# Optimization experiments

Measured on AMD Instinct MI355X. Metric: run time of the kernel, lower is better.

## Reference

```python
import jax, jax.numpy as jnp
import numpy as np

NUM_HEADS = 8
NEG_INF = -1e9  # stand-in for -inf in the causal mask (avoids nan under masked softmax)


def setup_inputs() -> dict:
    key = jax.random.key(0)
    ks = jax.random.split(key, 8)
    B, C, H, W = 2, 512, 64, 64
    E = 512
    s = 1.0 / np.sqrt(C)
    return {
        "query": jax.random.normal(ks[0], (B, C, H, W), jnp.float32),
        "key": jax.random.normal(ks[1], (B, C, H, W), jnp.float32),
        "Wq": jax.random.normal(ks[2], (E, C), jnp.float32) * s,
        "bq": jax.random.normal(ks[3], (E,), jnp.float32) * 0.01,
        "Wk": jax.random.normal(ks[4], (E, C), jnp.float32) * s,
        "bk": jax.random.normal(ks[5], (E,), jnp.float32) * 0.01,
        "Wv": jax.random.normal(ks[6], (E, C), jnp.float32) * s,
        "bv": jax.random.normal(ks[7], (E,), jnp.float32) * 0.01,
    }


def reference(query, key, Wq, bq, Wk, bk, Wv, bv):
    B, qdim, H, W = query.shape
    N = H * W
    E = Wq.shape[0]
    nh = NUM_HEADS
    hd = E // nh

    # (B, C, H, W) -> (B, N, C)
    q_tok = query.transpose(0, 2, 3, 1).reshape(B, N, qdim)
    k_tok = key.transpose(0, 2, 3, 1).reshape(B, N, key.shape[1])

    q = (q_tok @ Wq.T + bq).reshape(B, N, nh, hd)
    k = (k_tok @ Wk.T + bk).reshape(B, N, nh, hd)
    v = (k_tok @ Wv.T + bv).reshape(B, N, nh, hd)

    # scores: (B, heads, N, N)
    scores = jnp.einsum("bqhd,bkhd->bhqk", q, k) / jnp.sqrt(jnp.float32(hd))
    causal = jnp.tril(jnp.ones((N, N), dtype=bool))
    scores = jnp.where(causal, scores, NEG_INF)
    attn = jax.nn.softmax(scores, axis=-1)  # dropout p=0.0 -> identity

    x = jnp.einsum("bhqk,bkhd->bhqd", attn, v)  # (B, h, N, hd)
    # permute to (B, h, hd, N) then view as (B, E, H, W) — matches torch ordering
    out = x.transpose(0, 1, 3, 2).reshape(B, E, H, W)
    return out
```

## Files before the change

### kernel.cpp

```cpp
#include <hip/hip_runtime.h>


typedef __bf16 bf16;
typedef __attribute__((ext_vector_type(8))) __bf16 bf16x8;
typedef __attribute__((ext_vector_type(4))) float floatx4;

#define B_ 2
#define Cc 512
#define Nn 4096
#define Ee 512
#define NH 8
#define HD 64

#define QSCALE 0.1803368801111204f

__global__ __launch_bounds__(64) void detect_dtype(
    const unsigned short* __restrict__ w, int* __restrict__ flag) {
  bool bad = false;
#pragma unroll
  for (int i = 0; i < 16; ++i) {
    unsigned u = w[threadIdx.x * 16 + i];
    float v = __uint_as_float(u << 16);
    bad |= !(v > -1024.f && v < 1024.f);
  }
  unsigned long long b = __ballot(bad);
  if (threadIdx.x == 0) *flag = (b != 0ull) ? 1 : 0;
}

#define WSEG 262144
#define WTOT 787968
__global__ __launch_bounds__(256) void wcvt(
    const float* __restrict__ Wq, const float* __restrict__ Wk,
    const float* __restrict__ Wv, const float* __restrict__ bq,
    const float* __restrict__ bk, const float* __restrict__ bv,
    bf16* __restrict__ out, const int* __restrict__ flagp) {
  if (!*flagp) return;
  int idx = (blockIdx.x * 256 + threadIdx.x) * 8;
  if (idx >= WTOT) return;
  const float* src;
  int off;
  if (idx < WSEG)            { src = Wq; off = idx; }
  else if (idx < 2 * WSEG)   { src = Wk; off = idx - WSEG; }
  else if (idx < 3 * WSEG)   { src = Wv; off = idx - 2 * WSEG; }
  else if (idx < 3 * WSEG + 512)  { src = bq; off = idx - 3 * WSEG; }
  else if (idx < 3 * WSEG + 1024) { src = bk; off = idx - 3 * WSEG - 512; }
  else                            { src = bv; off = idx - 3 * WSEG - 1024; }
  float4 a = *(const float4*)(src + off);
  float4 c = *(const float4*)(src + off + 4);
  union { bf16 h[8]; bf16x8 v; } u;
  u.h[0] = (bf16)a.x; u.h[1] = (bf16)a.y; u.h[2] = (bf16)a.z; u.h[3] = (bf16)a.w;
  u.h[4] = (bf16)c.x; u.h[5] = (bf16)c.y; u.h[6] = (bf16)c.z; u.h[7] = (bf16)c.w;
  *(bf16x8*)(out + idx) = u.v;
}

__device__ __forceinline__ bf16x8 load8e(const void* base, size_t eidx, int f32) {
  if (!f32) return *(const bf16x8*)((const bf16*)base + eidx);
  const float* f = (const float*)base + eidx;
  float4 a = *(const float4*)f;
  float4 c = *(const float4*)(f + 4);
  union { bf16 h[8]; bf16x8 v; } u;
  u.h[0] = (bf16)a.x; u.h[1] = (bf16)a.y; u.h[2] = (bf16)a.z; u.h[3] = (bf16)a.w;
  u.h[4] = (bf16)c.x; u.h[5] = (bf16)c.y; u.h[6] = (bf16)c.z; u.h[7] = (bf16)c.w;
  return u.v;
}

__global__ __launch_bounds__(256) void transpose_k(
    const void* __restrict__ X0, const void* __restrict__ X1,
    bf16* __restrict__ T0, bf16* __restrict__ T1,
    const int* __restrict__ flagp) {
  const int f32 = *flagp;
  __shared__ __align__(16) bf16 T[64 * 64];
  const int z = blockIdx.z;
  const int bb = z & 1;
  const void* src = (z >> 1) ? X1 : X0;
  bf16* dst = (z >> 1) ? T1 : T0;
  const int n0 = blockIdx.x * 64, c0 = blockIdx.y * 64;
  const int t = threadIdx.x;
  const size_t sbase = ((size_t)bb * Cc + c0) * (size_t)Nn + n0;

#pragma unroll
  for (int it = 0; it < 2; ++it) {
    int task = t + it * 256;
    int crow = task >> 3, gr = task & 7;
    bf16x8 v = load8e(src, sbase + (size_t)crow * Nn + gr * 8, f32);
    int slot = gr ^ (crow & 7);
    *(bf16x8*)&T[crow * 64 + slot * 8] = v;
  }
  __syncthreads();
  const int nrow = t & 63, cp = t >> 6;
  bf16* db = dst + ((size_t)bb * Nn + n0 + nrow) * Cc + c0;
#pragma unroll
  for (int it = 0; it < 2; ++it) {
    int cg = cp * 2 + it;
    union { bf16 h[8]; bf16x8 v; } u;
#pragma unroll
    for (int j = 0; j < 8; ++j) {
      int c = cg * 8 + j;
      int slot = (nrow >> 3) ^ (c & 7);
      u.h[j] = T[c * 64 + slot * 8 + (nrow & 7)];
    }
    *(bf16x8*)(db + cg * 8) = u.v;
  }
}

__global__ __launch_bounds__(256) void gemm3(
    const bf16* __restrict__ Xtq, const bf16* __restrict__ Xtk,
    const void* __restrict__ Wq0, const bf16* __restrict__ Wqb,
    const void* __restrict__ Wk0, const bf16* __restrict__ Wkb,
    const void* __restrict__ Wv0, const bf16* __restrict__ Wvb,
    const void* __restrict__ bq0, const bf16* __restrict__ bqb,
    const void* __restrict__ bk0, const bf16* __restrict__ bkb,
    const void* __restrict__ bv0, const bf16* __restrict__ bvb,
    bf16* __restrict__ Qt, bf16* __restrict__ Kt, bf16* __restrict__ Vh,
    int zoff, const int* __restrict__ flagp) {
  const int f32 = *flagp;
  const int z = (int)blockIdx.z + zoff;
  const int op = z >> 1, b = z & 1;
  const bf16 *A, *Bt, *bias;
  bf16* Out;
  long sAb, sBb, sOb;
  int Nq, biasOnM, m0, n0;
  float scaleOut;
  if (op == 0) {
    A = Xtq; sAb = (long)Nn * Cc;
    Bt = f32 ? Wqb : (const bf16*)Wq0; sBb = 0;
    bias = f32 ? bqb : (const bf16*)bq0;
    Out = Qt; sOb = (long)Nn * Ee; Nq = Ee; biasOnM = 0; scaleOut = QSCALE;
    m0 = blockIdx.x * 128; n0 = blockIdx.y * 64;
  } else if (op == 1) {
    A = Xtk; sAb = (long)Nn * Cc;
    Bt = f32 ? Wkb : (const bf16*)Wk0; sBb = 0;
    bias = f32 ? bkb : (const bf16*)bk0;
    Out = Kt; sOb = (long)Nn * Ee; Nq = Ee; biasOnM = 0; scaleOut = 1.0f;
    m0 = blockIdx.x * 128; n0 = blockIdx.y * 64;
  } else {
    A = f32 ? Wvb : (const bf16*)Wv0; sAb = 0;
    Bt = Xtk; sBb = (long)Nn * Cc;
    bias = f32 ? bvb : (const bf16*)bv0;
    Out = Vh; sOb = (long)Ee * Nn; Nq = Nn; biasOnM = 1; scaleOut = 1.0f;
    m0 = (blockIdx.x >> 3) * 128;
    n0 = (blockIdx.y * 8 + (blockIdx.x & 7)) * 64;
  }
  constexpr int K = 512;
  constexpr int SA = 40;
  __shared__ __align__(16) bf16 As[2][128 * SA];
  __shared__ __align__(16) bf16 Bs[2][64 * SA];
  const int tid = threadIdx.x;
  const int lane = tid & 63, wave = tid >> 6;
  const int quad = lane >> 4, lm = lane & 15;
  const bf16* Ab = A + (size_t)b * sAb;
  const bf16* Bb = Bt + (size_t)b * sBb;
  bf16* Ob = Out + (size_t)b * sOb;

  const int arow = tid >> 2, ag = tid & 3;

  floatx4 acc[2][4];
#pragma unroll
  for (int i = 0; i < 2; ++i)
#pragma unroll
    for (int j = 0; j < 4; ++j) acc[i][j] = (floatx4){0.f, 0.f, 0.f, 0.f};

  bf16x8 a0 = *(const bf16x8*)(Ab + (size_t)(m0 + arow) * K + ag * 8);
  bf16x8 a1 = *(const bf16x8*)(Ab + (size_t)(m0 + 64 + arow) * K + ag * 8);
  bf16x8 b0 = *(const bf16x8*)(Bb + (size_t)(n0 + arow) * K + ag * 8);
  *(bf16x8*)&As[0][arow * SA + ag * 8] = a0;
  *(bf16x8*)&As[0][(64 + arow) * SA + ag * 8] = a1;
  *(bf16x8*)&Bs[0][arow * SA + ag * 8] = b0;
  __syncthreads();

  for (int kk = 0; kk < 16; ++kk) {
    const int c = kk & 1;
    const bool more = kk < 15;
    if (more) {
      int k0 = (kk + 1) * 32;
      a0 = *(const bf16x8*)(Ab + (size_t)(m0 + arow) * K + k0 + ag * 8);
      a1 = *(const bf16x8*)(Ab + (size_t)(m0 + 64 + arow) * K + k0 + ag * 8);
      b0 = *(const bf16x8*)(Bb + (size_t)(n0 + arow) * K + k0 + ag * 8);
    }
    bf16x8 af[2], bfr[4];
#pragma unroll
    for (int mf = 0; mf < 2; ++mf) {
      int r = wave * 32 + mf * 16 + lm;
      af[mf] = *(const bf16x8*)&As[c][r * SA + quad * 8];
    }
#pragma unroll
    for (int nf = 0; nf < 4; ++nf) {
      int r = nf * 16 + lm;
      bfr[nf] = *(const bf16x8*)&Bs[c][r * SA + quad * 8];
    }
    if (more) {
      *(bf16x8*)&As[c ^ 1][arow * SA + ag * 8] = a0;
      *(bf16x8*)&As[c ^ 1][(64 + arow) * SA + ag * 8] = a1;
      *(bf16x8*)&Bs[c ^ 1][arow * SA + ag * 8] = b0;
    }
#pragma unroll
    for (int mf = 0; mf < 2; ++mf)
#pragma unroll
      for (int nf = 0; nf < 4; ++nf)
        acc[mf][nf] = __builtin_amdgcn_mfma_f32_16x16x32_bf16(
            af[mf], bfr[nf], acc[mf][nf], 0, 0, 0);
    __syncthreads();
  }

#pragma unroll
  for (int mf = 0; mf < 2; ++mf) {
#pragma unroll
    for (int nf = 0; nf < 4; ++nf) {
      int col = n0 + nf * 16 + lm;
      float bn = biasOnM ? 0.f : (float)bias[col];
#pragma unroll
      for (int r = 0; r < 4; ++r) {
        int rowg = m0 + wave * 32 + mf * 16 + quad * 4 + r;
        float bv = biasOnM ? (float)bias[rowg] : bn;
        Ob[(size_t)rowg * Nq + col] = (bf16)((acc[mf][nf][r] + bv) * scaleOut);
      }
    }
  }
}

__device__ __forceinline__ float fast_exp2(float x) {
  return __builtin_amdgcn_exp2f(x);
}
__device__ __forceinline__ unsigned pack_bf16_2(float a, float b) {
  unsigned ua = __float_as_uint(a) + 0x8000u;
  unsigned ub = __float_as_uint(b) + 0x8000u;
  return (ua >> 16) | (ub & 0xFFFF0000u);
}

__global__ __launch_bounds__(256, 4) void attn(
    const bf16* __restrict__ Qt, const bf16* __restrict__ Kt,
    const bf16* __restrict__ Ve, void* __restrict__ Out,
    const int* __restrict__ flagp) {
  const int f32 = *flagp;
  constexpr int SK = 72;
  __shared__ __align__(16) bf16 Ks[2][64 * SK];
  __shared__ __align__(16) bf16 Vs[2][64 * SK];
  const int tid = threadIdx.x, lane = tid & 63, w = tid >> 6;
  const int quad = lane >> 4, lm = lane & 15;

  const int L = (int)blockIdx.x + 64 * (int)blockIdx.y + 512 * (int)blockIdx.z;
  const int xcd = L & 7, slot0 = L >> 3;
  const int half = slot0 >> 6, sp = slot0 & 63;
  const int p = half ? 63 - sp : sp;
  const int hp = xcd * 2 + half;
  const int b = hp >> 3, h = hp & 7;

  const int Q0 = p * 64;
  const int qbase = Q0 + w * 16;
  const int last = p;

  bf16x8 qf[2];
  {
    const bf16* qp =
        Qt + ((size_t)b * Nn + qbase + lm) * Ee + h * HD + quad * 8;
    qf[0] = *(const bf16x8*)qp;
    qf[1] = *(const bf16x8*)(qp + 32);
  }
  floatx4 accO[4];
#pragma unroll
  for (int df = 0; df < 4; ++df) accO[df] = (floatx4){0.f, 0.f, 0.f, 0.f};
  float lsum = 0.f;

  const int r0 = tid >> 3, g = tid & 7;
  const int sslot = ((g + r0) & 7) * 8;
  const bf16* kp0 = Kt + ((size_t)b * Nn + r0) * Ee + h * HD + g * 8;
  const bf16* kp1 = kp0 + (size_t)32 * Ee;
  const bf16* vp0 = Ve + ((size_t)b * Ee + h * HD + r0) * Nn + g * 8;
  const bf16* vp1 = vp0 + (size_t)32 * Nn;

  const int rbase = ((lm >> 2) << 3) | (lm & 3);

  bf16x8 ka[2], kb[2], va[2], vb[2];
#define LOADT(s)                                                   \
  do {                                                             \
    ka[s] = *(const bf16x8*)kp0; kb[s] = *(const bf16x8*)kp1;      \
    va[s] = *(const bf16x8*)vp0; vb[s] = *(const bf16x8*)vp1;      \
    kp0 += (size_t)64 * Ee; kp1 += (size_t)64 * Ee;                \
    vp0 += 64; vp1 += 64;                                          \
  } while (0)
#define STAGET(s, buf)                                             \
  do {                                                             \
    *(bf16x8*)&Ks[buf][r0 * SK + sslot] = ka[s];                   \
    *(bf16x8*)&Ks[buf][(r0 + 32) * SK + sslot] = kb[s];            \
    *(bf16x8*)&Vs[buf][r0 * SK + sslot] = va[s];                   \
    *(bf16x8*)&Vs[buf][(r0 + 32) * SK + sslot] = vb[s];            \
  } while (0)

  LOADT(0);
  if (last >= 1) LOADT(1);
  STAGET(0, 0);
  __syncthreads();

#pragma unroll 1
  for (int kt = 0; kt <= last; kt += 2) {
#pragma unroll
    for (int u = 0; u < 2; ++u) {
      const int t = kt + u;
      if (u == 1 && t > last) break;
      const int k0 = t * 64;
      if (t + 2 <= last) LOADT(u);
      const bool skip = k0 > qbase + 15;

      bf16x8 pb[2];
      if (!skip) {
        floatx4 accS[4];
#pragma unroll
        for (int f = 0; f < 4; ++f) accS[f] = (floatx4){0.f, 0.f, 0.f, 0.f};
        __builtin_amdgcn_s_setprio(1);
#pragma unroll
        for (int ks = 0; ks < 2; ++ks)
#pragma unroll
          for (int f = 0; f < 4; ++f) {
            const int R = rbase + ((f & 1) << 2) + ((f >> 1) << 5);
            const int sl = (ks * 4 + quad + R) & 7;
            bf16x8 ak = *(const bf16x8*)&Ks[u][R * SK + sl * 8];
            accS[f] = __builtin_amdgcn_mfma_f32_16x16x32_bf16(
                ak, qf[ks], accS[f], 0, 0, 0);
          }
        __builtin_amdgcn_s_setprio(0);
        const bool maskt = (k0 + 63 > qbase);
        if (!maskt) {
          float la = 0.f, lb = 0.f;
#pragma unroll
          for (int g2 = 0; g2 < 2; ++g2) {
            union { unsigned pk[4]; bf16x8 v; } uu;
#pragma unroll
            for (int jp = 0; jp < 4; ++jp) {
              const int fidx = g2 * 2 + (jp >> 1);
              const int re = (jp & 1) * 2;
              float p0 = fast_exp2(accS[fidx][re]);
              float p1 = fast_exp2(accS[fidx][re + 1]);
              la += p0; lb += p1;
              uu.pk[jp] = pack_bf16_2(p0, p1);
            }
            pb[g2] = uu.v;
          }
          lsum += la + lb;
        } else {
          const int qg = qbase + lm;
          float la = 0.f, lb = 0.f;
#pragma unroll
          for (int g2 = 0; g2 < 2; ++g2) {
            union { unsigned pk[4]; bf16x8 v; } uu;
#pragma unroll
            for (int jp = 0; jp < 4; ++jp) {
              const int fidx = g2 * 2 + (jp >> 1);
              const int re = (jp & 1) * 2;
              const int key0 = k0 + g2 * 32 + quad * 8 + jp * 2;
              float p0 = fast_exp2(accS[fidx][re]);
              float p1 = fast_exp2(accS[fidx][re + 1]);
              if (key0 > qg) p0 = 0.f;
              if (key0 + 1 > qg) p1 = 0.f;
              la += p0; lb += p1;
              uu.pk[jp] = pack_bf16_2(p0, p1);
            }
            pb[g2] = uu.v;
          }
          lsum += la + lb;
        }
      }
      if (t + 1 <= last) STAGET(u ^ 1, u ^ 1);
      if (!skip) {
        __builtin_amdgcn_s_setprio(1);
#pragma unroll
        for (int g2 = 0; g2 < 2; ++g2)
#pragma unroll
          for (int df = 0; df < 4; ++df) {
            const int Rv = df * 16 + lm;
            const int sl = (g2 * 4 + quad + Rv) & 7;
            bf16x8 av = *(const bf16x8*)&Vs[u][Rv * SK + sl * 8];
            accO[df] = __builtin_amdgcn_mfma_f32_16x16x32_bf16(
                av, pb[g2], accO[df], 0, 0, 0);
          }
        __builtin_amdgcn_s_setprio(0);
      }
      __syncthreads();
    }
  }
#undef LOADT
#undef STAGET

  lsum += __shfl_xor(lsum, 16);
  lsum += __shfl_xor(lsum, 32);

  const float inv = 1.0f / lsum;
  const int qg = qbase + lm;
#pragma unroll
  for (int df = 0; df < 4; ++df) {
#pragma unroll
    for (int r = 0; r < 4; ++r) {
      int d = h * HD + df * 16 + quad * 4 + r;
      size_t off = ((size_t)b * Ee + d) * Nn + qg;
      if (!f32) ((bf16*)Out)[off] = (bf16)(accO[df][r] * inv);
      else      ((float*)Out)[off] = accO[df][r] * inv;
    }
  }
}

extern "C" void kernel_launch(void* const* d_in, const int* in_sizes, int n_in,
                              void* d_out, int out_size, void* d_ws,
                              size_t ws_size, hipStream_t stream) {
  const void* q  = d_in[0];
  const void* k  = d_in[1];
  const void* Wq = d_in[2];
  const void* bq = d_in[3];
  const void* Wk = d_in[4];
  const void* bk = d_in[5];
  const void* Wv = d_in[6];
  const void* bv = d_in[7];

  const size_t SZ = (size_t)B_ * Nn * Cc;
  int*  flag = (int*)d_ws;
  bf16* Xtq  = (bf16*)((char*)d_ws + 1024);
  bf16* Qt   = Xtq + SZ;
  bf16* Kt   = Qt + SZ;
  bf16* Xtk  = (bf16*)d_out;
  bf16* Vh   = Xtq;
  bf16* Wb   = (bf16*)((char*)d_out + 8 * 1024 * 1024);
  bf16* Wqb = Wb,            *Wkb = Wb + WSEG,    *Wvb = Wb + 2 * WSEG;
  bf16* bqb = Wb + 3 * WSEG, *bkb = bqb + 512,    *bvb = bqb + 1024;

  detect_dtype<<<1, 64, 0, stream>>>((const unsigned short*)Wq, flag);
  wcvt<<<(WTOT / 8 + 255) / 256, 256, 0, stream>>>(
      (const float*)Wq, (const float*)Wk, (const float*)Wv,
      (const float*)bq, (const float*)bk, (const float*)bv, Wb, flag);
  transpose_k<<<dim3(64, 8, 4), 256, 0, stream>>>(q, k, Xtq, Xtk, flag);
  gemm3<<<dim3(32, 8, 4), 256, 0, stream>>>(
      Xtq, Xtk, Wq, Wqb, Wk, Wkb, Wv, Wvb,
      bq, bqb, bk, bkb, bv, bvb, Qt, Kt, Vh, 0, flag);
  gemm3<<<dim3(32, 8, 2), 256, 0, stream>>>(
      Xtq, Xtk, Wq, Wqb, Wk, Wkb, Wv, Wvb,
      bq, bqb, bk, bkb, bv, bvb, Qt, Kt, Vh, 4, flag);
  attn<<<dim3(64, NH, B_), 256, 0, stream>>>(Qt, Kt, Vh, d_out, flag);
}
```

Baseline: 191.6 us.

## Load V fragments directly from global into registers, drop V shared-memory staging

The attention kernel no longer stages V tiles through double-buffered shared memory. Each wave now loads its own V MFMA operands straight from global memory into registers at the start of each key tile. This removes the LDS writes and reads for V and halves shared memory use, which may allow higher occupancy. In exchange, each of the four waves redundantly fetches the full V tile from global/L2, and the load latency is only partly hidden by the QK and softmax work.

```diff
diff --git a/kernel.cpp b/kernel.cpp
--- a/kernel.cpp
+++ b/kernel.cpp
@@ -234,7 +234,6 @@
   const int f32 = *flagp;
   constexpr int SK = 72;
   __shared__ __align__(16) bf16 Ks[2][64 * SK];
-  __shared__ __align__(16) bf16 Vs[2][64 * SK];
   const int tid = threadIdx.x, lane = tid & 63, w = tid >> 6;
   const int quad = lane >> 4, lm = lane & 15;
 
@@ -265,30 +264,29 @@
   const int sslot = ((g + r0) & 7) * 8;
   const bf16* kp0 = Kt + ((size_t)b * Nn + r0) * Ee + h * HD + g * 8;
   const bf16* kp1 = kp0 + (size_t)32 * Ee;
-  const bf16* vp0 = Ve + ((size_t)b * Ee + h * HD + r0) * Nn + g * 8;
-  const bf16* vp1 = vp0 + (size_t)32 * Nn;
+
+  const bf16* vr0 = Ve + ((size_t)b * Ee + h * HD + lm) * Nn + quad * 8;
+  const bf16* vr1 = vr0 + (size_t)16 * Nn;
+  const bf16* vr2 = vr0 + (size_t)32 * Nn;
+  const bf16* vr3 = vr0 + (size_t)48 * Nn;
 
   const int rbase = ((lm >> 2) << 3) | (lm & 3);
 
-  bf16x8 ka[2], kb[2], va[2], vb[2];
-#define LOADT(s)                                                   \
+  bf16x8 ka[2], kb[2];
+#define LOADK(s)                                                   \
   do {                                                             \
     ka[s] = *(const bf16x8*)kp0; kb[s] = *(const bf16x8*)kp1;      \
-    va[s] = *(const bf16x8*)vp0; vb[s] = *(const bf16x8*)vp1;      \
     kp0 += (size_t)64 * Ee; kp1 += (size_t)64 * Ee;                \
-    vp0 += 64; vp1 += 64;                                          \
   } while (0)
-#define STAGET(s, buf)                                             \
+#define STAGEK(s, buf)                                             \
   do {                                                             \
     *(bf16x8*)&Ks[buf][r0 * SK + sslot] = ka[s];                   \
     *(bf16x8*)&Ks[buf][(r0 + 32) * SK + sslot] = kb[s];            \
-    *(bf16x8*)&Vs[buf][r0 * SK + sslot] = va[s];                   \
-    *(bf16x8*)&Vs[buf][(r0 + 32) * SK + sslot] = vb[s];            \
   } while (0)
 
-  LOADT(0);
-  if (last >= 1) LOADT(1);
-  STAGET(0, 0);
+  LOADK(0);
+  if (last >= 1) LOADK(1);
+  STAGEK(0, 0);
   __syncthreads();
 
 #pragma unroll 1
@@ -298,8 +296,18 @@
       const int t = kt + u;
       if (u == 1 && t > last) break;
       const int k0 = t * 64;
-      if (t + 2 <= last) LOADT(u);
       const bool skip = k0 > qbase + 15;
+
+      bf16x8 av0, av1, av2, av3, av4, av5, av6, av7;
+      if (!skip) {
+        av0 = *(const bf16x8*)(vr0);        av1 = *(const bf16x8*)(vr0 + 32);
+        av2 = *(const bf16x8*)(vr1);        av3 = *(const bf16x8*)(vr1 + 32);
+        av4 = *(const bf16x8*)(vr2);        av5 = *(const bf16x8*)(vr2 + 32);
+        av6 = *(const bf16x8*)(vr3);        av7 = *(const bf16x8*)(vr3 + 32);
+      }
+      vr0 += 64; vr1 += 64; vr2 += 64; vr3 += 64;
+
+      if (t + 2 <= last) LOADK(u);
 
       bf16x8 pb[2];
       if (!skip) {
@@ -359,26 +367,24 @@
           lsum += la + lb;
         }
       }
-      if (t + 1 <= last) STAGET(u ^ 1, u ^ 1);
+      if (t + 1 <= last) STAGEK(u ^ 1, u ^ 1);
       if (!skip) {
         __builtin_amdgcn_s_setprio(1);
-#pragma unroll
-        for (int g2 = 0; g2 < 2; ++g2)
-#pragma unroll
-          for (int df = 0; df < 4; ++df) {
-            const int Rv = df * 16 + lm;
-            const int sl = (g2 * 4 + quad + Rv) & 7;
-            bf16x8 av = *(const bf16x8*)&Vs[u][Rv * SK + sl * 8];
-            accO[df] = __builtin_amdgcn_mfma_f32_16x16x32_bf16(
-                av, pb[g2], accO[df], 0, 0, 0);
-          }
+        accO[0] = __builtin_amdgcn_mfma_f32_16x16x32_bf16(av0, pb[0], accO[0], 0, 0, 0);
+        accO[1] = __builtin_amdgcn_mfma_f32_16x16x32_bf16(av2, pb[0], accO[1], 0, 0, 0);
+        accO[2] = __builtin_amdgcn_mfma_f32_16x16x32_bf16(av4, pb[0], accO[2], 0, 0, 0);
+        accO[3] = __builtin_amdgcn_mfma_f32_16x16x32_bf16(av6, pb[0], accO[3], 0, 0, 0);
+        accO[0] = __builtin_amdgcn_mfma_f32_16x16x32_bf16(av1, pb[1], accO[0], 0, 0, 0);
+        accO[1] = __builtin_amdgcn_mfma_f32_16x16x32_bf16(av3, pb[1], accO[1], 0, 0, 0);
+        accO[2] = __builtin_amdgcn_mfma_f32_16x16x32_bf16(av5, pb[1], accO[2], 0, 0, 0);
+        accO[3] = __builtin_amdgcn_mfma_f32_16x16x32_bf16(av7, pb[1], accO[3], 0, 0, 0);
         __builtin_amdgcn_s_setprio(0);
       }
       __syncthreads();
     }
   }
-#undef LOADT
-#undef STAGET
+#undef LOADK
+#undef STAGEK
 
   lsum += __shfl_xor(lsum, 16);
   lsum += __shfl_xor(lsum, 32);
```

Measured after the change: 266.3 us. 1.39x slower.

## Software-pipeline QK^T one tile ahead of softmax and PV in attention

Applied to the files above, without the earlier changes.

Restructures the causal attention loop so the score MFMAs for tile t+1 are issued before the exp and PV MFMAs of tile t, using two score accumulator sets. K is staged two tiles ahead and V one tile ahead, with clamped prefetch indices so loads run unconditionally. It also drops the per-wave skip check for fully masked tiles. The aim is to overlap MFMA work with the exp/pack ALU work and to hide memory latency, at the cost of more registers and possibly lower occupancy.

```diff
diff --git a/kernel.cpp b/kernel.cpp
--- a/kernel.cpp
+++ b/kernel.cpp
@@ -227,6 +227,89 @@
   return (ua >> 16) | (ub & 0xFFFF0000u);
 }
 
+#define TCLMP(tt) ((tt) > 63 ? 63 : (tt))
+
+#define ATTN_STEP(t_, u_, CUR, NXT)                                          \
+  {                                                                          \
+       \
+    *(bf16x8*)&Ks[(u_)][r0 * SK + sslot] = ka[(u_)];                         \
+    *(bf16x8*)&Ks[(u_)][(r0 + 32) * SK + sslot] = kb[(u_)];                  \
+    *(bf16x8*)&Vs[(u_) ^ 1][r0 * SK + sslot] = va[(u_)];                     \
+    *(bf16x8*)&Vs[(u_) ^ 1][(r0 + 32) * SK + sslot] = vb[(u_)];              \
+                                       \
+    ka[(u_)] = *(const bf16x8*)(kp0 + (size_t)TCLMP((t_) + 4) * (64 * Ee));  \
+    kb[(u_)] = *(const bf16x8*)(kp1 + (size_t)TCLMP((t_) + 4) * (64 * Ee));  \
+    va[(u_)] = *(const bf16x8*)(vp0 + TCLMP((t_) + 3) * 64);                 \
+    vb[(u_)] = *(const bf16x8*)(vp1 + TCLMP((t_) + 3) * 64);                 \
+                 \
+    if ((t_) < last) {                                                       \
+      _Pragma("unroll") for (int f = 0; f < 4; ++f)                          \
+          NXT[f] = (floatx4){0.f, 0.f, 0.f, 0.f};                            \
+      __builtin_amdgcn_s_setprio(1);                                         \
+      _Pragma("unroll") for (int ks2 = 0; ks2 < 2; ++ks2) {                  \
+        _Pragma("unroll") for (int f = 0; f < 4; ++f) {                      \
+          const int R = rbase + ((f & 1) << 2) + ((f >> 1) << 5);            \
+          const int sl = (ks2 * 4 + quad + R) & 7;                           \
+          bf16x8 ak = *(const bf16x8*)&Ks[(u_) ^ 1][R * SK + sl * 8];        \
+          NXT[f] = __builtin_amdgcn_mfma_f32_16x16x32_bf16(                  \
+              ak, qf[ks2], NXT[f], 0, 0, 0);                                 \
+        }                                                                    \
+      }                                                                      \
+      __builtin_amdgcn_s_setprio(0);                                         \
+    }                                                                        \
+                        \
+    bf16x8 pb[2];                                                            \
+    if ((t_) != last) {                                                      \
+      float la = 0.f, lb = 0.f;                                              \
+      _Pragma("unroll") for (int g2 = 0; g2 < 2; ++g2) {                     \
+        union { unsigned pk[4]; bf16x8 v; } uu;                              \
+        _Pragma("unroll") for (int jp = 0; jp < 4; ++jp) {                   \
+          const int fidx = g2 * 2 + (jp >> 1);                               \
+          const int re = (jp & 1) * 2;                                       \
+          float p0 = fast_exp2(CUR[fidx][re]);                               \
+          float p1 = fast_exp2(CUR[fidx][re + 1]);                           \
+          la += p0; lb += p1;                                                \
+          uu.pk[jp] = pack_bf16_2(p0, p1);                                   \
+        }                                                                    \
+        pb[g2] = uu.v;                                                       \
+      }                                                                      \
+      lsum += la + lb;                                                       \
+    } else {                                                                 \
+      const int qgm = qbase + lm;                                            \
+      const int k0b = (t_) * 64;                                             \
+      float la = 0.f, lb = 0.f;                                              \
+      _Pragma("unroll") for (int g2 = 0; g2 < 2; ++g2) {                     \
+        union { unsigned pk[4]; bf16x8 v; } uu;                              \
+        _Pragma("unroll") for (int jp = 0; jp < 4; ++jp) {                   \
+          const int fidx = g2 * 2 + (jp >> 1);                               \
+          const int re = (jp & 1) * 2;                                       \
+          const int key0 = k0b + g2 * 32 + quad * 8 + jp * 2;                \
+          float p0 = fast_exp2(CUR[fidx][re]);                               \
+          float p1 = fast_exp2(CUR[fidx][re + 1]);                           \
+          if (key0 > qgm) p0 = 0.f;                                          \
+          if (key0 + 1 > qgm) p1 = 0.f;                                      \
+          la += p0; lb += p1;                                                \
+          uu.pk[jp] = pack_bf16_2(p0, p1);                                   \
+        }                                                                    \
+        pb[g2] = uu.v;                                                       \
+      }                                                                      \
+      lsum += la + lb;                                                       \
+    }                                                                        \
+                                                       \
+    __builtin_amdgcn_s_setprio(1);                                           \
+    _Pragma("unroll") for (int g2 = 0; g2 < 2; ++g2) {                       \
+      _Pragma("unroll") for (int df = 0; df < 4; ++df) {                     \
+        const int Rv = df * 16 + lm;                                         \
+        const int sl = (g2 * 4 + quad + Rv) & 7;                             \
+        bf16x8 av = *(const bf16x8*)&Vs[(u_)][Rv * SK + sl * 8];             \
+        accO[df] = __builtin_amdgcn_mfma_f32_16x16x32_bf16(                  \
+            av, pb[g2], accO[df], 0, 0, 0);                                  \
+      }                                                                      \
+    }                                                                        \
+    __builtin_amdgcn_s_setprio(0);                                           \
+    __syncthreads();                                                         \
+  }
+
 __global__ __launch_bounds__(256, 4) void attn(
     const bf16* __restrict__ Qt, const bf16* __restrict__ Kt,
     const bf16* __restrict__ Ve, void* __restrict__ Out,
@@ -245,8 +328,7 @@
   const int hp = xcd * 2 + half;
   const int b = hp >> 3, h = hp & 7;
 
-  const int Q0 = p * 64;
-  const int qbase = Q0 + w * 16;
+  const int qbase = p * 64 + w * 16;
   const int last = p;
 
   bf16x8 qf[2];
@@ -271,114 +353,54 @@
   const int rbase = ((lm >> 2) << 3) | (lm & 3);
 
   bf16x8 ka[2], kb[2], va[2], vb[2];
-#define LOADT(s)                                                   \
-  do {                                                             \
-    ka[s] = *(const bf16x8*)kp0; kb[s] = *(const bf16x8*)kp1;      \
-    va[s] = *(const bf16x8*)vp0; vb[s] = *(const bf16x8*)vp1;      \
-    kp0 += (size_t)64 * Ee; kp1 += (size_t)64 * Ee;                \
-    vp0 += 64; vp1 += 64;                                          \
-  } while (0)
-#define STAGET(s, buf)                                             \
-  do {                                                             \
-    *(bf16x8*)&Ks[buf][r0 * SK + sslot] = ka[s];                   \
-    *(bf16x8*)&Ks[buf][(r0 + 32) * SK + sslot] = kb[s];            \
-    *(bf16x8*)&Vs[buf][r0 * SK + sslot] = va[s];                   \
-    *(bf16x8*)&Vs[buf][(r0 + 32) * SK + sslot] = vb[s];            \
-  } while (0)
-
-  LOADT(0);
-  if (last >= 1) LOADT(1);
-  STAGET(0, 0);
+
+  ka[0] = *(const bf16x8*)kp0;
+  kb[0] = *(const bf16x8*)kp1;
+  ka[1] = *(const bf16x8*)(kp0 + (size_t)64 * Ee);
+  kb[1] = *(const bf16x8*)(kp1 + (size_t)64 * Ee);
+  va[0] = *(const bf16x8*)vp0;
+  vb[0] = *(const bf16x8*)vp1;
+  *(bf16x8*)&Ks[0][r0 * SK + sslot] = ka[0];
+  *(bf16x8*)&Ks[0][(r0 + 32) * SK + sslot] = kb[0];
+  *(bf16x8*)&Ks[1][r0 * SK + sslot] = ka[1];
+  *(bf16x8*)&Ks[1][(r0 + 32) * SK + sslot] = kb[1];
+  *(bf16x8*)&Vs[0][r0 * SK + sslot] = va[0];
+  *(bf16x8*)&Vs[0][(r0 + 32) * SK + sslot] = vb[0];
+  ka[0] = *(const bf16x8*)(kp0 + (size_t)2 * 64 * Ee);
+  kb[0] = *(const bf16x8*)(kp1 + (size_t)2 * 64 * Ee);
+  ka[1] = *(const bf16x8*)(kp0 + (size_t)3 * 64 * Ee);
+  kb[1] = *(const bf16x8*)(kp1 + (size_t)3 * 64 * Ee);
+  va[0] = *(const bf16x8*)(vp0 + 1 * 64);
+  vb[0] = *(const bf16x8*)(vp1 + 1 * 64);
+  va[1] = *(const bf16x8*)(vp0 + 2 * 64);
+  vb[1] = *(const bf16x8*)(vp1 + 2 * 64);
   __syncthreads();
+
+  floatx4 accSA[4], accSB[4];
+#pragma unroll
+  for (int f = 0; f < 4; ++f) {
+    accSA[f] = (floatx4){0.f, 0.f, 0.f, 0.f};
+    accSB[f] = (floatx4){0.f, 0.f, 0.f, 0.f};
+  }
+  __builtin_amdgcn_s_setprio(1);
+#pragma unroll
+  for (int ks2 = 0; ks2 < 2; ++ks2) {
+#pragma unroll
+    for (int f = 0; f < 4; ++f) {
+      const int R = rbase + ((f & 1) << 2) + ((f >> 1) << 5);
+      const int sl = (ks2 * 4 + quad + R) & 7;
+      bf16x8 ak = *(const bf16x8*)&Ks[0][R * SK + sl * 8];
+      accSA[f] = __builtin_amdgcn_mfma_f32_16x16x32_bf16(
+          ak, qf[ks2], accSA[f], 0, 0, 0);
+    }
+  }
+  __builtin_amdgcn_s_setprio(0);
 
 #pragma unroll 1
   for (int kt = 0; kt <= last; kt += 2) {
-#pragma unroll
-    for (int u = 0; u < 2; ++u) {
-      const int t = kt + u;
-      if (u == 1 && t > last) break;
-      const int k0 = t * 64;
-      if (t + 2 <= last) LOADT(u);
-      const bool skip = k0 > qbase + 15;
-
-      bf16x8 pb[2];
-      if (!skip) {
-        floatx4 accS[4];
-#pragma unroll
-        for (int f = 0; f < 4; ++f) accS[f] = (floatx4){0.f, 0.f, 0.f, 0.f};
-        __builtin_amdgcn_s_setprio(1);
-#pragma unroll
-        for (int ks = 0; ks < 2; ++ks)
-#pragma unroll
-          for (int f = 0; f < 4; ++f) {
-            const int R = rbase + ((f & 1) << 2) + ((f >> 1) << 5);
-            const int sl = (ks * 4 + quad + R) & 7;
-            bf16x8 ak = *(const bf16x8*)&Ks[u][R * SK + sl * 8];
-            accS[f] = __builtin_amdgcn_mfma_f32_16x16x32_bf16(
-                ak, qf[ks], accS[f], 0, 0, 0);
-          }
-        __builtin_amdgcn_s_setprio(0);
-        const bool maskt = (k0 + 63 > qbase);
-        if (!maskt) {
-          float la = 0.f, lb = 0.f;
-#pragma unroll
-          for (int g2 = 0; g2 < 2; ++g2) {
-            union { unsigned pk[4]; bf16x8 v; } uu;
-#pragma unroll
-            for (int jp = 0; jp < 4; ++jp) {
-              const int fidx = g2 * 2 + (jp >> 1);
-              const int re = (jp & 1) * 2;
-              float p0 = fast_exp2(accS[fidx][re]);
-              float p1 = fast_exp2(accS[fidx][re + 1]);
-              la += p0; lb += p1;
-              uu.pk[jp] = pack_bf16_2(p0, p1);
-            }
-            pb[g2] = uu.v;
-          }
-          lsum += la + lb;
-        } else {
-          const int qg = qbase + lm;
-          float la = 0.f, lb = 0.f;
-#pragma unroll
-          for (int g2 = 0; g2 < 2; ++g2) {
-            union { unsigned pk[4]; bf16x8 v; } uu;
-#pragma unroll
-            for (int jp = 0; jp < 4; ++jp) {
-              const int fidx = g2 * 2 + (jp >> 1);
-              const int re = (jp & 1) * 2;
-              const int key0 = k0 + g2 * 32 + quad * 8 + jp * 2;
-              float p0 = fast_exp2(accS[fidx][re]);
-              float p1 = fast_exp2(accS[fidx][re + 1]);
-              if (key0 > qg) p0 = 0.f;
-              if (key0 + 1 > qg) p1 = 0.f;
-              la += p0; lb += p1;
-              uu.pk[jp] = pack_bf16_2(p0, p1);
-            }
-            pb[g2] = uu.v;
-          }
-          lsum += la + lb;
-        }
-      }
-      if (t + 1 <= last) STAGET(u ^ 1, u ^ 1);
-      if (!skip) {
-        __builtin_amdgcn_s_setprio(1);
-#pragma unroll
-        for (int g2 = 0; g2 < 2; ++g2)
-#pragma unroll
-          for (int df = 0; df < 4; ++df) {
-            const int Rv = df * 16 + lm;
-            const int sl = (g2 * 4 + quad + Rv) & 7;
-            bf16x8 av = *(const bf16x8*)&Vs[u][Rv * SK + sl * 8];
-            accO[df] = __builtin_amdgcn_mfma_f32_16x16x32_bf16(
-                av, pb[g2], accO[df], 0, 0, 0);
-          }
-        __builtin_amdgcn_s_setprio(0);
-      }
-      __syncthreads();
-    }
-  }
-#undef LOADT
-#undef STAGET
+    ATTN_STEP(kt, 0, accSA, accSB);
+    if (kt + 1 <= last) ATTN_STEP(kt + 1, 1, accSB, accSA);
+  }
 
   lsum += __shfl_xor(lsum, 16);
   lsum += __shfl_xor(lsum, 32);
```

Result: slower. 255.6 us (+33.4%).

## Fuse weight conversion into transpose, merge projection GEMMs, deepen GEMM prefetch

Applied to the files above, without the earlier changes.

Folds the weight/bias bf16 conversion into the input-transpose kernel as an extra grid slice, so one launch replaces two. When the workspace is large enough, V gets its own buffer instead of aliasing the transposed query, which lets all three projections run in a single GEMM launch. The GEMM main loop now prefetches global tiles two steps ahead using register double-buffering. These changes cut launch and serialization overhead and hide more load latency, at the cost of extra registers and workspace memory.

```diff
diff --git a/kernel.cpp b/kernel.cpp
--- a/kernel.cpp
+++ b/kernel.cpp
@@ -29,29 +29,6 @@
 
 #define WSEG 262144
 #define WTOT 787968
-__global__ __launch_bounds__(256) void wcvt(
-    const float* __restrict__ Wq, const float* __restrict__ Wk,
-    const float* __restrict__ Wv, const float* __restrict__ bq,
-    const float* __restrict__ bk, const float* __restrict__ bv,
-    bf16* __restrict__ out, const int* __restrict__ flagp) {
-  if (!*flagp) return;
-  int idx = (blockIdx.x * 256 + threadIdx.x) * 8;
-  if (idx >= WTOT) return;
-  const float* src;
-  int off;
-  if (idx < WSEG)            { src = Wq; off = idx; }
-  else if (idx < 2 * WSEG)   { src = Wk; off = idx - WSEG; }
-  else if (idx < 3 * WSEG)   { src = Wv; off = idx - 2 * WSEG; }
-  else if (idx < 3 * WSEG + 512)  { src = bq; off = idx - 3 * WSEG; }
-  else if (idx < 3 * WSEG + 1024) { src = bk; off = idx - 3 * WSEG - 512; }
-  else                            { src = bv; off = idx - 3 * WSEG - 1024; }
-  float4 a = *(const float4*)(src + off);
-  float4 c = *(const float4*)(src + off + 4);
-  union { bf16 h[8]; bf16x8 v; } u;
-  u.h[0] = (bf16)a.x; u.h[1] = (bf16)a.y; u.h[2] = (bf16)a.z; u.h[3] = (bf16)a.w;
-  u.h[4] = (bf16)c.x; u.h[5] = (bf16)c.y; u.h[6] = (bf16)c.z; u.h[7] = (bf16)c.w;
-  *(bf16x8*)(out + idx) = u.v;
-}
 
 __device__ __forceinline__ bf16x8 load8e(const void* base, size_t eidx, int f32) {
   if (!f32) return *(const bf16x8*)((const bf16*)base + eidx);
@@ -64,11 +41,35 @@
   return u.v;
 }
 
-__global__ __launch_bounds__(256) void transpose_k(
+__global__ __launch_bounds__(256) void prep(
     const void* __restrict__ X0, const void* __restrict__ X1,
     bf16* __restrict__ T0, bf16* __restrict__ T1,
-    const int* __restrict__ flagp) {
+    const float* __restrict__ Wq, const float* __restrict__ Wk,
+    const float* __restrict__ Wv, const float* __restrict__ bq,
+    const float* __restrict__ bk, const float* __restrict__ bv,
+    bf16* __restrict__ Wb, const int* __restrict__ flagp) {
   const int f32 = *flagp;
+  if (blockIdx.z == 4) {
+    if (!f32) return;
+    int task = (int)blockIdx.y * 64 + (int)blockIdx.x;
+    int idx = (task * 256 + (int)threadIdx.x) * 8;
+    if (idx >= WTOT) return;
+    const float* src;
+    int off;
+    if (idx < WSEG)            { src = Wq; off = idx; }
+    else if (idx < 2 * WSEG)   { src = Wk; off = idx - WSEG; }
+    else if (idx < 3 * WSEG)   { src = Wv; off = idx - 2 * WSEG; }
+    else if (idx < 3 * WSEG + 512)  { src = bq; off = idx - 3 * WSEG; }
+    else if (idx < 3 * WSEG + 1024) { src = bk; off = idx - 3 * WSEG - 512; }
+    else                            { src = bv; off = idx - 3 * WSEG - 1024; }
+    float4 a = *(const float4*)(src + off);
+    float4 c = *(const float4*)(src + off + 4);
+    union { bf16 h[8]; bf16x8 v; } u;
+    u.h[0] = (bf16)a.x; u.h[1] = (bf16)a.y; u.h[2] = (bf16)a.z; u.h[3] = (bf16)a.w;
+    u.h[4] = (bf16)c.x; u.h[5] = (bf16)c.y; u.h[6] = (bf16)c.z; u.h[7] = (bf16)c.w;
+    *(bf16x8*)(Wb + idx) = u.v;
+    return;
+  }
   __shared__ __align__(16) bf16 T[64 * 64];
   const int z = blockIdx.z;
   const int bb = z & 1;
@@ -160,47 +161,54 @@
 #pragma unroll
     for (int j = 0; j < 4; ++j) acc[i][j] = (floatx4){0.f, 0.f, 0.f, 0.f};
 
-  bf16x8 a0 = *(const bf16x8*)(Ab + (size_t)(m0 + arow) * K + ag * 8);
-  bf16x8 a1 = *(const bf16x8*)(Ab + (size_t)(m0 + 64 + arow) * K + ag * 8);
-  bf16x8 b0 = *(const bf16x8*)(Bb + (size_t)(n0 + arow) * K + ag * 8);
-  *(bf16x8*)&As[0][arow * SA + ag * 8] = a0;
-  *(bf16x8*)&As[0][(64 + arow) * SA + ag * 8] = a1;
-  *(bf16x8*)&Bs[0][arow * SA + ag * 8] = b0;
+  bf16x8 pa0[2], pa1[2], pb0[2];
+#define LOADG(s, step)                                                      \
+  do {                                                                      \
+    const int k0_ = (step) * 32;                                            \
+    pa0[s] = *(const bf16x8*)(Ab + (size_t)(m0 + arow) * K + k0_ + ag * 8); \
+    pa1[s] = *(const bf16x8*)(Ab + (size_t)(m0 + 64 + arow) * K + k0_ + ag * 8); \
+    pb0[s] = *(const bf16x8*)(Bb + (size_t)(n0 + arow) * K + k0_ + ag * 8); \
+  } while (0)
+#define STAGEG(s, c_)                                                       \
+  do {                                                                      \
+    *(bf16x8*)&As[c_][arow * SA + ag * 8] = pa0[s];                         \
+    *(bf16x8*)&As[c_][(64 + arow) * SA + ag * 8] = pa1[s];                  \
+    *(bf16x8*)&Bs[c_][arow * SA + ag * 8] = pb0[s];                         \
+  } while (0)
+
+  LOADG(0, 0);
+  LOADG(1, 1);
+  STAGEG(0, 0);
   __syncthreads();
 
-  for (int kk = 0; kk < 16; ++kk) {
-    const int c = kk & 1;
-    const bool more = kk < 15;
-    if (more) {
-      int k0 = (kk + 1) * 32;
-      a0 = *(const bf16x8*)(Ab + (size_t)(m0 + arow) * K + k0 + ag * 8);
-      a1 = *(const bf16x8*)(Ab + (size_t)(m0 + 64 + arow) * K + k0 + ag * 8);
-      b0 = *(const bf16x8*)(Bb + (size_t)(n0 + arow) * K + k0 + ag * 8);
+  for (int kk = 0; kk < 16; kk += 2) {
+#pragma unroll
+    for (int u = 0; u < 2; ++u) {
+      const int t = kk + u;
+      if (t + 2 < 16) LOADG(u, t + 2);
+      bf16x8 af[2], bfr[4];
+#pragma unroll
+      for (int mf = 0; mf < 2; ++mf) {
+        int r = wave * 32 + mf * 16 + lm;
+        af[mf] = *(const bf16x8*)&As[u][r * SA + quad * 8];
+      }
+#pragma unroll
+      for (int nf = 0; nf < 4; ++nf) {
+        int r = nf * 16 + lm;
+        bfr[nf] = *(const bf16x8*)&Bs[u][r * SA + quad * 8];
+      }
+      if (t + 1 < 16) STAGEG(u ^ 1, u ^ 1);
+#pragma unroll
+      for (int mf = 0; mf < 2; ++mf)
+#pragma unroll
+        for (int nf = 0; nf < 4; ++nf)
+          acc[mf][nf] = __builtin_amdgcn_mfma_f32_16x16x32_bf16(
+              af[mf], bfr[nf], acc[mf][nf], 0, 0, 0);
+      __syncthreads();
     }
-    bf16x8 af[2], bfr[4];
-#pragma unroll
-    for (int mf = 0; mf < 2; ++mf) {
-      int r = wave * 32 + mf * 16 + lm;
-      af[mf] = *(const bf16x8*)&As[c][r * SA + quad * 8];
-    }
-#pragma unroll
-    for (int nf = 0; nf < 4; ++nf) {
-      int r = nf * 16 + lm;
-      bfr[nf] = *(const bf16x8*)&Bs[c][r * SA + quad * 8];
-    }
-    if (more) {
-      *(bf16x8*)&As[c ^ 1][arow * SA + ag * 8] = a0;
-      *(bf16x8*)&As[c ^ 1][(64 + arow) * SA + ag * 8] = a1;
-      *(bf16x8*)&Bs[c ^ 1][arow * SA + ag * 8] = b0;
-    }
-#pragma unroll
-    for (int mf = 0; mf < 2; ++mf)
-#pragma unroll
-      for (int nf = 0; nf < 4; ++nf)
-        acc[mf][nf] = __builtin_amdgcn_mfma_f32_16x16x32_bf16(
-            af[mf], bfr[nf], acc[mf][nf], 0, 0, 0);
-    __syncthreads();
-  }
+  }
+#undef LOADG
+#undef STAGEG
 
 #pragma unroll
   for (int mf = 0; mf < 2; ++mf) {
@@ -415,21 +423,30 @@
   bf16* Qt   = Xtq + SZ;
   bf16* Kt   = Qt + SZ;
   bf16* Xtk  = (bf16*)d_out;
-  bf16* Vh   = Xtq;
   bf16* Wb   = (bf16*)((char*)d_out + 8 * 1024 * 1024);
   bf16* Wqb = Wb,            *Wkb = Wb + WSEG,    *Wvb = Wb + 2 * WSEG;
   bf16* bqb = Wb + 3 * WSEG, *bkb = bqb + 512,    *bvb = bqb + 1024;
 
+  const size_t need = 1024 + 4 * SZ * sizeof(bf16);
+  const bool sep = ws_size >= need;
+  bf16* Vh = sep ? (Kt + SZ) : Xtq;
+
   detect_dtype<<<1, 64, 0, stream>>>((const unsigned short*)Wq, flag);
-  wcvt<<<(WTOT / 8 + 255) / 256, 256, 0, stream>>>(
+  prep<<<dim3(64, 8, 5), 256, 0, stream>>>(
+      q, k, Xtq, Xtk,
       (const float*)Wq, (const float*)Wk, (const float*)Wv,
       (const float*)bq, (const float*)bk, (const float*)bv, Wb, flag);
-  transpose_k<<<dim3(64, 8, 4), 256, 0, stream>>>(q, k, Xtq, Xtk, flag);
-  gemm3<<<dim3(32, 8, 4), 256, 0, stream>>>(
-      Xtq, Xtk, Wq, Wqb, Wk, Wkb, Wv, Wvb,
-      bq, bqb, bk, bkb, bv, bvb, Qt, Kt, Vh, 0, flag);
-  gemm3<<<dim3(32, 8, 2), 256, 0, stream>>>(
-      Xtq, Xtk, Wq, Wqb, Wk, Wkb, Wv, Wvb,
-      bq, bqb, bk, bkb, bv, bvb, Qt, Kt, Vh, 4, flag);
+  if (sep) {
+    gemm3<<<dim3(32, 8, 6), 256, 0, stream>>>(
+        Xtq, Xtk, Wq, Wqb, Wk, Wkb, Wv, Wvb,
+        bq, bqb, bk, bkb, bv, bvb, Qt, Kt, Vh, 0, flag);
+  } else {
+    gemm3<<<dim3(32, 8, 4), 256, 0, stream>>>(
+        Xtq, Xtk, Wq, Wqb, Wk, Wkb, Wv, Wvb,
+        bq, bqb, bk, bkb, bv, bvb, Qt, Kt, Vh, 0, flag);
+    gemm3<<<dim3(32, 8, 2), 256, 0, stream>>>(
+        Xtq, Xtk, Wq, Wqb, Wk, Wkb, Wv, Wvb,
+        bq, bqb, bk, bkb, bv, bvb, Qt, Kt, Vh, 4, flag);
+  }
   attn<<<dim3(64, NH, B_), 256, 0, stream>>>(Qt, Kt, Vh, d_out, flag);
 }
```

Result: faster. 177.1 us (-7.5%).
